# Kernel tuning notes

Hardware: AMD Instinct MI355X
Metric: run time of the kernel (lower is better)

Reference implementation:

```python
import jax, jax.numpy as jnp
import numpy as np

H_DIM = 64
GRID = 8
NS = 2.0  # neighborhood_size
S = 256   # number of sequences (scenes)
P = 64    # pedestrians per sequence
EPS = 1e-5


def setup_inputs() -> dict:
    key = jax.random.key(0)
    k = jax.random.split(key, 6)
    N = S * P
    G = GRID * GRID
    h_states = jax.random.normal(k[0], (1, N, H_DIM), jnp.float32)
    end_pos = jax.random.normal(k[1], (N, 2), jnp.float32)
    starts = (jnp.arange(S, dtype=jnp.int32) * P)
    seq_start_end = jnp.stack([starts, starts + P], axis=1)  # (S, 2)
    # mlp_pool: Linear(G*H_DIM -> H_DIM) + BatchNorm1d + ReLU
    W = jax.random.normal(k[2], (G * H_DIM, H_DIM), jnp.float32) / np.sqrt(G * H_DIM)
    b = jnp.zeros((H_DIM,), jnp.float32)
    gamma = jnp.ones((H_DIM,), jnp.float32)
    beta = jnp.zeros((H_DIM,), jnp.float32)
    return {"h_states": h_states, "seq_start_end": seq_start_end, "end_pos": end_pos,
            "W": W, "b": b, "gamma": gamma, "beta": beta}


def reference(h_states, seq_start_end, end_pos, W, b, gamma, beta):
    nseq = seq_start_end.shape[0]          # S (static)
    N = end_pos.shape[0]
    Hd = h_states.shape[-1]
    nped = N // nseq                       # P (static; equal-length sequences)
    G = GRID * GRID
    half = NS / 2.0

    h = h_states.reshape(N, Hd).reshape(nseq, nped, Hd)     # (S, P, H)
    pos = end_pos.reshape(nseq, nped, 2)                    # (S, P, 2)

    # bounds per center pedestrian i
    tl_x = pos[..., 0] - half   # (S, P)
    tl_y = pos[..., 1] + half
    br_x = pos[..., 0] + half
    br_y = pos[..., 1] - half

    # pairwise: axis 1 = center i, axis 2 = other k
    ox = pos[:, None, :, 0]     # (S, 1, P)
    oy = pos[:, None, :, 1]
    cell_x = jnp.floor((ox - tl_x[:, :, None]) / NS * GRID)
    cell_y = jnp.floor((tl_y[:, :, None] - oy) / NS * GRID)
    grid = cell_x + cell_y * GRID                            # (S, P, P)

    oob = ((ox >= br_x[:, :, None]) | (ox <= tl_x[:, :, None]) |
           (oy >= tl_y[:, :, None]) | (oy <= br_y[:, :, None]))
    diag = jnp.eye(nped, dtype=bool)[None]                   # self excluded (within_bound[0::P+1]=1)
    valid = (~oob) & (~diag)

    grid_i = jnp.clip(grid.astype(jnp.int32), 0, G - 1)      # masked entries don't matter
    seq_off = (jnp.arange(nseq, dtype=jnp.int32)[:, None, None] * nped
               + jnp.arange(nped, dtype=jnp.int32)[None, :, None]) * G
    dummy = nseq * nped * G
    ids = jnp.where(valid, seq_off + grid_i, dummy)          # (S, P, P)

    # data for (s, i, k) is hidden of other k (curr_hidden.repeat(num_ped, 1))
    data = jnp.broadcast_to(h[:, None, :, :], (nseq, nped, nped, Hd)).reshape(-1, Hd)
    pooled = jax.ops.segment_sum(data, ids.reshape(-1), num_segments=dummy + 1)[:-1]
    x = pooled.reshape(N, G * Hd)                            # (N, G*H), row i = concat over grid cells

    # mlp_pool: Linear -> BatchNorm1d (train mode, biased var) -> ReLU
    x = x @ W + b
    mu = jnp.mean(x, axis=0)
    var = jnp.mean((x - mu) ** 2, axis=0)
    x = gamma * (x - mu) / jnp.sqrt(var + EPS) + beta
    return jnp.maximum(x, 0.0)
```

## Files before the change

### kernel.cpp

```cpp
#include <hip/hip_runtime.h>
#include <hip/hip_bf16.h>


#define NSEQ 256
#define NTOT (NSEQ*64)
#define EPSV 1e-5f

typedef __attribute__((ext_vector_type(8))) short short8;
typedef __attribute__((ext_vector_type(4))) float f32x4;
typedef unsigned short ushort_t;

__device__ __forceinline__ ushort_t f2b(float f) {
    __hip_bfloat16 h = __float2bfloat16(f);
    return *reinterpret_cast<ushort_t*>(&h);
}
__device__ __forceinline__ int kperm(int k) {
    return ((k >> 5)*2 + ((k & 7) >> 2))*16 + ((k >> 3) & 3)*4 + (k & 3);
}

__global__ __launch_bounds__(256) void sp_transpose(
    const float* __restrict__ W, short* __restrict__ Wt)
{
    __shared__ __align__(16) float Tl[64*68];
    const int b = blockIdx.x, tid = threadIdx.x;
    const float* wg = W + (size_t)b*4096;
    for (int m = 0; m < 4; ++m) {
        int c = m*256 + tid;
        int k = c >> 4, t0 = (c & 15)*4;
        *(f32x4*)(Tl + k*68 + t0) = *(const f32x4*)(wg + k*64 + t0);
    }
    __syncthreads();
    for (int m = 0; m < 2; ++m) {
        int q = m*256 + tid;
        int col = q >> 3, k0 = (q & 7)*8;
        short8 o;
        #pragma unroll
        for (int i2 = 0; i2 < 8; ++i2)
            o[i2] = (short)f2b(Tl[kperm(k0 + i2)*68 + col]);
        *(short8*)(Wt + ((size_t)(b*64 + col)*64 + k0)) = o;
    }
}

#define SM_CM   9216
#define SM_POS  13312
#define SM_XS1  17408
#define SM_RED  34816
#define SM_TOT  36864

__global__ __launch_bounds__(512, 2) void sp_main(
    const float* __restrict__ h, const float* __restrict__ pos,
    const short* __restrict__ Wt, const float* __restrict__ bvec,
    float* __restrict__ X, float* __restrict__ partials)
{
    __shared__ __align__(16) char smem[SM_TOT];
    ushort_t*      Ht = (ushort_t*)(smem);
    unsigned char* cm = (unsigned char*)(smem + SM_CM);
    float*         px = (float*)(smem + SM_POS);
    float*         py = px + 64;

    const int b    = blockIdx.x;
    const int base = b * 64;
    const int tid  = threadIdx.x;
    const int lane = tid & 63, w = tid >> 6;
    const int ln15 = lane & 15, ln4 = lane >> 4;
    const int xph  = (b >> 3) & 7;

    if (tid < 64) { px[tid] = pos[(base + tid)*2]; py[tid] = pos[(base + tid)*2 + 1]; }
    for (int m = 0; m < 2; ++m) {
        int c = m*512 + tid;
        int j = c >> 4, t0 = (c & 15)*4;
        f32x4 v = *(const f32x4*)(h + (size_t)(base + j)*64 + t0);
        #pragma unroll
        for (int u = 0; u < 4; ++u) Ht[(t0 + u)*72 + j] = f2b(v[u]);
    }
    __syncthreads();

    for (int m = 0; m < 8; ++m) {
        int p = m*512 + tid;
        int i = p >> 6, j = p & 63;
        unsigned char val = 255;
        if (i != j) {
            float ax = px[i], ay = py[i], ox = px[j], oy = py[j];
            float tlx = ax - 1.0f, tly = ay + 1.0f, brx = ax + 1.0f, bry = ay - 1.0f;
            bool oob = (ox >= brx) | (ox <= tlx) | (oy >= tly) | (oy <= bry);
            if (!oob) {
                int g = (int)(floorf((ox - tlx)*4.0f) + floorf((tly - oy)*4.0f)*8.0f);
                g = g < 0 ? 0 : (g > 63 ? 63 : g);
                val = (unsigned char)g;
            }
        }
        cm[i*64 + j] = val;
    }
    __syncthreads();

    short8 hf2[4][2];
    #pragma unroll
    for (int mt = 0; mt < 4; ++mt)
        #pragma unroll
        for (int kt2 = 0; kt2 < 2; ++kt2)
            hf2[mt][kt2] = *(const short8*)(Ht + (mt*16 + ln15)*72 + kt2*32 + ln4*8);
    unsigned cmv[4][2][2];
    #pragma unroll
    for (int rt = 0; rt < 4; ++rt)
        #pragma unroll
        for (int kt = 0; kt < 2; ++kt) {
            const unsigned* cp = (const unsigned*)(cm + (rt*16 + ln15)*64 + kt*32 + ln4*8);
            cmv[rt][kt][0] = cp[0]; cmv[rt][kt][1] = cp[1];
        }

    f32x4 acc[4][4];
    #pragma unroll
    for (int rt = 0; rt < 4; ++rt)
        #pragma unroll
        for (int nt = 0; nt < 4; ++nt) acc[rt][nt] = (f32x4){0.f,0.f,0.f,0.f};

    auto load_cell = [&](short8 (&bw)[2][4], int cidx) {
        const int g = w*8 + ((cidx + xph) & 7);
        const short* wg = Wt + (size_t)g*4096;
        #pragma unroll
        for (int kt = 0; kt < 2; ++kt)
            #pragma unroll
            for (int nt = 0; nt < 4; ++nt)
                bw[kt][nt] = *(const short8*)(wg + (nt*16 + ln15)*64 + kt*32 + ln4*8);
    };
    auto compute_cell = [&](const short8 (&bw)[2][4], int cidx) {
        const int g = w*8 + ((cidx + xph) & 7);
        #pragma unroll
        for (int rt = 0; rt < 4; ++rt) {
            short8 sf[2];
            #pragma unroll
            for (int kt = 0; kt < 2; ++kt)
                #pragma unroll
                for (int u = 0; u < 8; ++u) {
                    unsigned byte = ((u < 4 ? cmv[rt][kt][0] >> (8*u)
                                           : cmv[rt][kt][1] >> (8*(u-4))) & 255u);
                    sf[kt][u] = (byte == (unsigned)g) ? (short)0x3F80 : (short)0;
                }
            f32x4 pt[4];
            #pragma unroll
            for (int mt = 0; mt < 4; ++mt) pt[mt] = (f32x4){0.f,0.f,0.f,0.f};
            #pragma unroll
            for (int kt2 = 0; kt2 < 2; ++kt2)
                #pragma unroll
                for (int mt = 0; mt < 4; ++mt)
                    pt[mt] = __builtin_amdgcn_mfma_f32_16x16x32_bf16(hf2[mt][kt2], sf[kt2], pt[mt], 0, 0, 0);
            #pragma unroll
            for (int kt = 0; kt < 2; ++kt) {
                short8 af;
                #pragma unroll
                for (int r = 0; r < 4; ++r) {
                    af[r]     = (short)f2b(pt[2*kt    ][r]);
                    af[4 + r] = (short)f2b(pt[2*kt + 1][r]);
                }
                #pragma unroll
                for (int nt = 0; nt < 4; ++nt)
                    acc[rt][nt] = __builtin_amdgcn_mfma_f32_16x16x32_bf16(af, bw[kt][nt], acc[rt][nt], 0, 0, 0);
            }
        }
    };

    short8 bwA[2][4], bwB[2][4];
    load_cell(bwA, 0);
    #pragma unroll
    for (int cc = 0; cc < 8; cc += 2) {
        if (cc + 1 < 8) load_cell(bwB, cc + 1);
        compute_cell(bwA, cc);
        if (cc + 2 < 8) load_cell(bwA, cc + 2);
        if (cc + 1 < 8) compute_cell(bwB, cc + 1);
    }
    __syncthreads();

    float* Xs0 = (float*)smem;
    float* Xs1 = (float*)(smem + SM_XS1);
    for (int step = 0; step < 4; ++step) {
        if ((w & 3) == step) {
            float* Xs = (w < 4) ? Xs0 : Xs1;
            #pragma unroll
            for (int rt = 0; rt < 4; ++rt)
                #pragma unroll
                for (int nt = 0; nt < 4; ++nt)
                    #pragma unroll
                    for (int r = 0; r < 4; ++r) {
                        int row = rt*16 + ln4*4 + r;
                        int col = nt*16 + ln15;
                        if (step == 0) Xs[row*68 + col]  = acc[rt][nt][r];
                        else           Xs[row*68 + col] += acc[rt][nt][r];
                    }
        }
        __syncthreads();
    }

    {
        const int row = tid >> 3, c0 = (tid & 7)*8;
        float* xg = X + (size_t)(base + row)*64 + c0;
        #pragma unroll
        for (int q = 0; q < 2; ++q) {
            f32x4 v;
            #pragma unroll
            for (int u = 0; u < 4; ++u) {
                int o = row*68 + c0 + q*4 + u;
                v[u] = Xs0[o] + Xs1[o] + bvec[c0 + q*4 + u];
            }
            *(f32x4*)(xg + q*4) = v;
        }
    }

    {
        float* red1 = (float*)(smem + SM_RED);
        float* red2 = red1 + 256;
        if (tid < 256) {
            int col = tid & 63, rg = tid >> 6;
            float bc = bvec[col], s1 = 0.f, s2 = 0.f;
            for (int ii = 0; ii < 16; ++ii) {
                int o = (rg*16 + ii)*68 + col;
                float xv = Xs0[o] + Xs1[o] + bc;
                s1 += xv; s2 += xv*xv;
            }
            red1[rg*64 + col] = s1;
            red2[rg*64 + col] = s2;
        }
        __syncthreads();
        if (tid < 128) {
            int hs = tid >> 6, c2 = tid & 63;
            const float* r0 = hs ? red2 : red1;
            float v = r0[c2] + r0[64 + c2] + r0[128 + c2] + r0[192 + c2];
            partials[(size_t)b*128 + hs*64 + c2] = v;
        }
    }
}

__global__ __launch_bounds__(256) void sp_finish(
    float* __restrict__ X, const float* __restrict__ partials,
    const float* __restrict__ gamma, const float* __restrict__ beta)
{
    __shared__ float sp0[128], sp1[128];
    __shared__ float scale[64], shift[64];
    const int b = blockIdx.x, tid = threadIdx.x;

    {
        const int slot = tid & 127, hb = tid >> 7;
        float v = 0.f;
        const float* p = partials + (size_t)hb*128*128 + slot;
        #pragma unroll 4
        for (int bb = 0; bb < 128; ++bb) v += p[(size_t)bb*128];
        (hb ? sp1 : sp0)[slot] = v;
    }
    __syncthreads();
    if (tid < 64) {
        const float inv_n = 1.0f / (float)NTOT;
        float s1 = sp0[tid] + sp1[tid];
        float s2 = sp0[64 + tid] + sp1[64 + tid];
        float mu  = s1 * inv_n;
        float var = s2 * inv_n - mu*mu;
        float sc  = gamma[tid] / sqrtf(var + EPSV);
        scale[tid] = sc;
        shift[tid] = beta[tid] - mu*sc;
    }
    __syncthreads();
    #pragma unroll
    for (int q = 0; q < 4; ++q) {
        size_t idx4 = (size_t)b*1024 + q*256 + tid;
        f32x4 v = ((f32x4*)X)[idx4];
        int c0 = ((int)idx4*4) & 63;
        #pragma unroll
        for (int u = 0; u < 4; ++u)
            v[u] = fmaxf(v[u]*scale[c0 + u] + shift[c0 + u], 0.0f);
        ((f32x4*)X)[idx4] = v;
    }
}

extern "C" void kernel_launch(void* const* d_in, const int* in_sizes, int n_in,
                              void* d_out, int out_size, void* d_ws, size_t ws_size,
                              hipStream_t stream)
{
    const float* h     = (const float*)d_in[0];
    const float* pos   = (const float*)d_in[2];
    const float* W     = (const float*)d_in[3];
    const float* bvec  = (const float*)d_in[4];
    const float* gamma = (const float*)d_in[5];
    const float* beta  = (const float*)d_in[6];

    float* X        = (float*)d_out;
    short* Wt       = (short*)d_ws;
    float* partials = (float*)((char*)d_ws + 524288);

    sp_transpose<<<64,   256, 0, stream>>>(W, Wt);
    sp_main     <<<NSEQ, 512, 0, stream>>>(h, pos, Wt, bvec, X, partials);
    sp_finish   <<<NSEQ, 256, 0, stream>>>(X, partials, gamma, beta);
}
```

Before: 104.1 us.

## Fuse transpose, main and finish kernels into one persistent kernel with global flags

After: 223.7 us. 2.15x slower.

```diff
diff --git a/kernel.cpp b/kernel.cpp
--- a/kernel.cpp
+++ b/kernel.cpp
@@ -18,45 +18,35 @@
     return ((k >> 5)*2 + ((k & 7) >> 2))*16 + ((k >> 3) & 3)*4 + (k & 3);
 }
 
-__global__ __launch_bounds__(256) void sp_transpose(
-    const float* __restrict__ W, short* __restrict__ Wt)
-{
-    __shared__ __align__(16) float Tl[64*68];
-    const int b = blockIdx.x, tid = threadIdx.x;
-    const float* wg = W + (size_t)b*4096;
-    for (int m = 0; m < 4; ++m) {
-        int c = m*256 + tid;
-        int k = c >> 4, t0 = (c & 15)*4;
-        *(f32x4*)(Tl + k*68 + t0) = *(const f32x4*)(wg + k*64 + t0);
-    }
-    __syncthreads();
-    for (int m = 0; m < 2; ++m) {
-        int q = m*256 + tid;
-        int col = q >> 3, k0 = (q & 7)*8;
-        short8 o;
-        #pragma unroll
-        for (int i2 = 0; i2 < 8; ++i2)
-            o[i2] = (short)f2b(Tl[kperm(k0 + i2)*68 + col]);
-        *(short8*)(Wt + ((size_t)(b*64 + col)*64 + k0)) = o;
-    }
-}
+#define WS_WT   0
+#define WS_PART 524288
+#define WS_GST  655360
+#define WS_FLG  656384
 
 #define SM_CM   9216
 #define SM_POS  13312
 #define SM_XS1  17408
 #define SM_RED  34816
-#define SM_TOT  36864
-
-__global__ __launch_bounds__(512, 2) void sp_main(
+#define SM_FLGL 36864
+#define SM_TOT  36880
+
+__global__ __launch_bounds__(512, 2) void sp_one(
     const float* __restrict__ h, const float* __restrict__ pos,
-    const short* __restrict__ Wt, const float* __restrict__ bvec,
-    float* __restrict__ X, float* __restrict__ partials)
+    const float* __restrict__ W, const float* __restrict__ bvec,
+    const float* __restrict__ gamma, const float* __restrict__ beta,
+    float* __restrict__ X, char* __restrict__ ws)
 {
+    short*    Wt       = (short*)(ws + WS_WT);
+    float*    partials = (float*)(ws + WS_PART);
+    float*    gstats   = (float*)(ws + WS_GST);
+    unsigned* flg      = (unsigned*)(ws + WS_FLG);
+
     __shared__ __align__(16) char smem[SM_TOT];
-    ushort_t*      Ht = (ushort_t*)(smem);
-    unsigned char* cm = (unsigned char*)(smem + SM_CM);
-    float*         px = (float*)(smem + SM_POS);
-    float*         py = px + 64;
+    ushort_t*      Ht     = (ushort_t*)(smem);
+    unsigned char* cm     = (unsigned char*)(smem + SM_CM);
+    float*         px     = (float*)(smem + SM_POS);
+    float*         py     = px + 64;
+    unsigned*      islast = (unsigned*)(smem + SM_FLGL);
 
     const int b    = blockIdx.x;
     const int base = b * 64;
@@ -64,6 +54,30 @@
     const int lane = tid & 63, w = tid >> 6;
     const int ln15 = lane & 15, ln4 = lane >> 4;
     const int xph  = (b >> 3) & 7;
+
+    if (b < 64) {
+        float* Tl = (float*)smem;
+        const float* wg = W + (size_t)b*4096;
+        #pragma unroll
+        for (int m = 0; m < 2; ++m) {
+            int c = m*512 + tid;
+            int k = c >> 4, t0 = (c & 15)*4;
+            *(f32x4*)(Tl + k*68 + t0) = *(const f32x4*)(wg + k*64 + t0);
+        }
+        __syncthreads();
+        {
+            int col = tid >> 3, k0 = (tid & 7)*8;
+            short8 o;
+            #pragma unroll
+            for (int i2 = 0; i2 < 8; ++i2)
+                o[i2] = (short)f2b(Tl[kperm(k0 + i2)*68 + col]);
+            *(short8*)(Wt + ((size_t)(b*64 + col)*64 + k0)) = o;
+        }
+        __threadfence();
+        __syncthreads();
+        if (tid == 0) atomicAdd(&flg[0], 1u);
+        __syncthreads();
+    }
 
     if (tid < 64) { px[tid] = pos[(base + tid)*2]; py[tid] = pos[(base + tid)*2 + 1]; }
     for (int m = 0; m < 2; ++m) {
@@ -114,6 +128,10 @@
         #pragma unroll
         for (int nt = 0; nt < 4; ++nt) acc[rt][nt] = (f32x4){0.f,0.f,0.f,0.f};
 
+    if (tid == 0) { while (atomicAdd(&flg[0], 0u) < 64u) __builtin_amdgcn_s_sleep(8); }
+    __syncthreads();
+    __threadfence();
+
     auto load_cell = [&](short8 (&bw)[2][4], int cidx) {
         const int g = w*8 + ((cidx + xph) & 7);
         const short* wg = Wt + (size_t)g*4096;
@@ -188,21 +206,6 @@
                     }
         }
         __syncthreads();
-    }
-
-    {
-        const int row = tid >> 3, c0 = (tid & 7)*8;
-        float* xg = X + (size_t)(base + row)*64 + c0;
-        #pragma unroll
-        for (int q = 0; q < 2; ++q) {
-            f32x4 v;
-            #pragma unroll
-            for (int u = 0; u < 4; ++u) {
-                int o = row*68 + c0 + q*4 + u;
-                v[u] = Xs0[o] + Xs1[o] + bvec[c0 + q*4 + u];
-            }
-            *(f32x4*)(xg + q*4) = v;
-        }
     }
 
     {
@@ -227,45 +230,60 @@
             partials[(size_t)b*128 + hs*64 + c2] = v;
         }
     }
-}
-
-__global__ __launch_bounds__(256) void sp_finish(
-    float* __restrict__ X, const float* __restrict__ partials,
-    const float* __restrict__ gamma, const float* __restrict__ beta)
-{
-    __shared__ float sp0[128], sp1[128];
-    __shared__ float scale[64], shift[64];
-    const int b = blockIdx.x, tid = threadIdx.x;
-
+    __threadfence();
+    __syncthreads();
+    if (tid == 0) *islast = (atomicAdd(&flg[1], 1u) == NSEQ - 1u) ? 1u : 0u;
+    __syncthreads();
+
+    if (*islast) {
+        __threadfence();
+        float* redsum = (float*)(smem + SM_RED);
+        const int slot = tid & 127, quarter = tid >> 7;
+        const volatile float* pp = partials;
+        float v = 0.f;
+        for (int bb = 0; bb < 64; ++bb)
+            v += pp[(size_t)(quarter*64 + bb)*128 + slot];
+        redsum[quarter*128 + slot] = v;
+        __syncthreads();
+        if (tid < 128) {
+            float t = redsum[tid] + redsum[128+tid] + redsum[256+tid] + redsum[384+tid];
+            redsum[tid] = t;
+        }
+        __syncthreads();
+        if (tid < 64) {
+            const float inv_n = 1.0f / (float)NTOT;
+            float mu  = redsum[tid] * inv_n;
+            float var = redsum[64 + tid] * inv_n - mu*mu;
+            float sc  = gamma[tid] / sqrtf(var + EPSV);
+            gstats[tid]      = sc;
+            gstats[64 + tid] = beta[tid] - mu*sc;
+        }
+        __threadfence();
+        __syncthreads();
+        if (tid == 0) atomicExch(&flg[2], 1u);
+    }
+
+    if (tid == 0) { while (atomicAdd(&flg[2], 0u) == 0u) __builtin_amdgcn_s_sleep(8); }
+    __syncthreads();
+    __threadfence();
+    float* scsh = (float*)(smem + SM_RED);
+    if (tid < 128) scsh[tid] = ((const volatile float*)gstats)[tid];
+    __syncthreads();
     {
-        const int slot = tid & 127, hb = tid >> 7;
-        float v = 0.f;
-        const float* p = partials + (size_t)hb*128*128 + slot;
-        #pragma unroll 4
-        for (int bb = 0; bb < 128; ++bb) v += p[(size_t)bb*128];
-        (hb ? sp1 : sp0)[slot] = v;
-    }
-    __syncthreads();
-    if (tid < 64) {
-        const float inv_n = 1.0f / (float)NTOT;
-        float s1 = sp0[tid] + sp1[tid];
-        float s2 = sp0[64 + tid] + sp1[64 + tid];
-        float mu  = s1 * inv_n;
-        float var = s2 * inv_n - mu*mu;
-        float sc  = gamma[tid] / sqrtf(var + EPSV);
-        scale[tid] = sc;
-        shift[tid] = beta[tid] - mu*sc;
-    }
-    __syncthreads();
-    #pragma unroll
-    for (int q = 0; q < 4; ++q) {
-        size_t idx4 = (size_t)b*1024 + q*256 + tid;
-        f32x4 v = ((f32x4*)X)[idx4];
-        int c0 = ((int)idx4*4) & 63;
-        #pragma unroll
-        for (int u = 0; u < 4; ++u)
-            v[u] = fmaxf(v[u]*scale[c0 + u] + shift[c0 + u], 0.0f);
-        ((f32x4*)X)[idx4] = v;
+        const int row = tid >> 3, c0 = (tid & 7)*8;
+        float* xg = X + (size_t)(base + row)*64 + c0;
+        #pragma unroll
+        for (int q = 0; q < 2; ++q) {
+            f32x4 v;
+            #pragma unroll
+            for (int u = 0; u < 4; ++u) {
+                int cc2 = c0 + q*4 + u;
+                int o   = row*68 + cc2;
+                float xv = Xs0[o] + Xs1[o] + bvec[cc2];
+                v[u] = fmaxf(xv*scsh[cc2] + scsh[64 + cc2], 0.0f);
+            }
+            *(f32x4*)(xg + q*4) = v;
+        }
     }
 }
 
@@ -280,11 +298,9 @@
     const float* gamma = (const float*)d_in[5];
     const float* beta  = (const float*)d_in[6];
 
-    float* X        = (float*)d_out;
-    short* Wt       = (short*)d_ws;
-    float* partials = (float*)((char*)d_ws + 524288);
-
-    sp_transpose<<<64,   256, 0, stream>>>(W, Wt);
-    sp_main     <<<NSEQ, 512, 0, stream>>>(h, pos, Wt, bvec, X, partials);
-    sp_finish   <<<NSEQ, 256, 0, stream>>>(X, partials, gamma, beta);
+    float* X  = (float*)d_out;
+    char*  ws = (char*)d_ws;
+
+    hipMemsetAsync(ws + WS_FLG, 0, 64, stream);
+    sp_one<<<NSEQ, 512, 0, stream>>>(h, pos, W, bvec, gamma, beta, X, ws);
 }
```
